# Kernel tuning notes

Measured on AMD Instinct MI355X. Metric: run time of the kernel, lower is better.

## Reference

```python
import jax, jax.numpy as jnp
import numpy as np

D_IN = 1024
D_OUT = 1024
NUM_HEADS = 16
HEAD_DIM = D_OUT // NUM_HEADS


def setup_inputs() -> dict:
    key = jax.random.key(0)
    k_x, k_qkv, k_pw, k_pb = jax.random.split(key, 4)
    x = jax.random.normal(k_x, (2, 2048, D_IN), dtype=jnp.float32)
    # torch nn.Linear(d_in, 3*d_out, bias=False): weight [3*d_out, d_in]
    w_qkv = jax.random.normal(k_qkv, (3 * D_OUT, D_IN), dtype=jnp.float32) * (1.0 / np.sqrt(D_IN))
    # proj: nn.Linear(d_out, d_out) with bias
    w_proj = jax.random.normal(k_pw, (D_OUT, D_OUT), dtype=jnp.float32) * (1.0 / np.sqrt(D_OUT))
    b_proj = jax.random.normal(k_pb, (D_OUT,), dtype=jnp.float32) * 0.01
    return {"x": x, "w_qkv": w_qkv, "w_proj": w_proj, "b_proj": b_proj}


def reference(x, w_qkv, w_proj, b_proj):
    B, S, _ = x.shape
    # fused QKV projection: [B,S,3*D_OUT]
    qkv = jnp.einsum('bsd,ed->bse', x, w_qkv)
    qkv = qkv.reshape(B, S, 3, NUM_HEADS, HEAD_DIM)
    q, k, v = jnp.moveaxis(qkv, 2, 0)  # each [B,S,H,Dh]
    scale = 1.0 / jnp.sqrt(jnp.asarray(HEAD_DIM, dtype=x.dtype))
    # scores [B,H,S,S]
    scores = jnp.einsum('bqhd,bkhd->bhqk', q, k) * scale
    causal = jnp.tril(jnp.ones((S, S), dtype=bool))
    scores = jnp.where(causal, scores, jnp.asarray(-jnp.inf, dtype=scores.dtype))
    attn = jax.nn.softmax(scores, axis=-1)
    ctx = jnp.einsum('bhqk,bkhd->bqhd', attn, v)  # [B,S,H,Dh]
    ctx = ctx.reshape(B, S, D_OUT)
    return jnp.einsum('bsd,ed->bse', ctx, w_proj) + b_proj
```

## Files before the change

### kernel.cpp

```cpp
#include <hip/hip_runtime.h>
#include <hip/hip_bf16.h>
#include <cstdint>

#define B_SZ   2
#define S_LEN  2048
#define NH     16
#define LDA    72

using f32x4 = __attribute__((ext_vector_type(4))) float;
typedef __bf16 bf16x8 __attribute__((ext_vector_type(8)));
typedef __bf16 bf16x4 __attribute__((ext_vector_type(4)));

__device__ inline float bf2f(unsigned short u) {
    union { unsigned int i; float f; } v; v.i = ((unsigned int)u) << 16; return v.f;
}
__device__ inline unsigned short f2bf(float f) {
    union { float f; unsigned int i; } v; v.f = f;
    unsigned int r = v.i + 0x7fff + ((v.i >> 16) & 1);
    return (unsigned short)(r >> 16);
}
__device__ inline f32x4 mfma16(bf16x8 a, bf16x8 b, f32x4 c) {
    return __builtin_amdgcn_mfma_f32_16x16x32_bf16(a, b, c, 0, 0, 0);
}
__device__ inline unsigned pack_bf16x2(float lo, float hi) {
    float2 f2; f2.x = lo; f2.y = hi;
    __hip_bfloat162 bb = __float22bfloat162_rn(f2);
    union { __hip_bfloat162 b; unsigned u; } cv; cv.b = bb;
    return cv.u;
}
__device__ inline void ldsbar() {
    __builtin_amdgcn_sched_barrier(0);
    asm volatile("s_waitcnt lgkmcnt(0)" ::: "memory");
    __builtin_amdgcn_s_barrier();
    __builtin_amdgcn_sched_barrier(0);
}
__device__ inline void stC(float* C, size_t idx, float v)  { C[idx] = v; }
__device__ inline void stC(__bf16* C, size_t idx, float v) { ((unsigned short*)C)[idx] = f2bf(v); }

#define QSF (0.125f * 1.4426950408889634f)

__global__ __launch_bounds__(256) void f2b3_kernel(
    const float* __restrict__ a, int na4, __bf16* __restrict__ outa,
    const float* __restrict__ b, int nb4, __bf16* __restrict__ outb,
    const float* __restrict__ c, int nc4, __bf16* __restrict__ outc)
{
    int i = blockIdx.x * blockDim.x + threadIdx.x;
    const float* src; __bf16* dst; int idx;
    if (i < na4)                  { src = a; dst = outa; idx = i; }
    else if (i < na4 + nb4)       { src = b; dst = outb; idx = i - na4; }
    else if (i < na4 + nb4 + nc4) { src = c; dst = outc; idx = i - na4 - nb4; }
    else return;
    float4 v = ((const float4*)src)[idx];
    ushort4 o;
    o.x = f2bf(v.x); o.y = f2bf(v.y); o.z = f2bf(v.z); o.w = f2bf(v.w);
    ((ushort4*)dst)[idx] = o;
}

template <typename TO, int HAS_BIAS, int QSCALE>
__global__ __launch_bounds__(256) void gemm128(
    const __bf16* __restrict__ A, const __bf16* __restrict__ W,
    const float* __restrict__ bias, TO* __restrict__ C,
    int M, int N, int K)
{
    __shared__ __bf16 Alds[3][128 * 32];
    __shared__ __bf16 Blds[3][128 * 32];
    const int tid  = threadIdx.x, lane = tid & 63, w = tid >> 6;
    const int c16  = lane & 15, quad = lane >> 4;
    const int mBase = blockIdx.y * 128, nBase = blockIdx.x * 128;
    const int moff = (w & 1) * 64, noff = (w >> 1) * 64;

    f32x4 acc[4][4];
#pragma unroll
    for (int i = 0; i < 4; ++i)
#pragma unroll
        for (int j = 0; j < 4; ++j) acc[i][j] = (f32x4){0.f, 0.f, 0.f, 0.f};

    auto stage = [&](int buf, int k0) {
#pragma unroll
        for (int p = 0; p < 2; ++p) {
            const int linear = p * 256 + tid;
            const int row = linear >> 2;
            const int seg = (linear & 3) ^ (row & 3);
            const int lbase = (p * 256 + w * 64) * 8;
            const __bf16* ga = A + (size_t)(mBase + row) * K + k0 + seg * 8;
            const __bf16* gb = W + (size_t)(nBase + row) * K + k0 + seg * 8;
            __builtin_amdgcn_global_load_lds(
                (const __attribute__((address_space(1))) void*)ga,
                (__attribute__((address_space(3))) void*)(&Alds[buf][lbase]), 16, 0, 0);
            __builtin_amdgcn_global_load_lds(
                (const __attribute__((address_space(1))) void*)gb,
                (__attribute__((address_space(3))) void*)(&Blds[buf][lbase]), 16, 0, 0);
        }
    };

    stage(0, 0);
    if (32 < K) stage(1, 32);
    int cur = 0;
    for (int k0 = 0; k0 < K; k0 += 32) {
        __builtin_amdgcn_sched_barrier(0);
        if (k0 + 32 < K) asm volatile("s_waitcnt vmcnt(4) lgkmcnt(0)" ::: "memory");
        else             asm volatile("s_waitcnt vmcnt(0) lgkmcnt(0)" ::: "memory");
        __builtin_amdgcn_s_barrier();
        __builtin_amdgcn_sched_barrier(0);

        if (k0 + 64 < K) stage(cur == 0 ? 2 : cur - 1, k0 + 64);

        bf16x8 af[4], bw[4];
#pragma unroll
        for (int i = 0; i < 4; ++i) {
            const int rowA = moff + i * 16 + c16;
            af[i] = *(const bf16x8*)&Alds[cur][rowA * 32 + ((quad ^ (rowA & 3)) << 3)];
            const int rowB = noff + i * 16 + c16;
            bw[i] = *(const bf16x8*)&Blds[cur][rowB * 32 + ((quad ^ (rowB & 3)) << 3)];
        }
#pragma unroll
        for (int i = 0; i < 4; ++i)
#pragma unroll
            for (int j = 0; j < 4; ++j)
                acc[i][j] = mfma16(af[i], bw[j], acc[i][j]);
        cur = (cur == 2) ? 0 : cur + 1;
    }

#pragma unroll
    for (int j = 0; j < 4; ++j) {
        const int colBase = nBase + noff + j * 16;
        const float qs = (QSCALE && colBase < 1024) ? QSF : 1.0f;
        const int col = colBase + c16;
        const float bv = HAS_BIAS ? bias[col] : 0.f;
#pragma unroll
        for (int i = 0; i < 4; ++i)
#pragma unroll
            for (int r = 0; r < 4; ++r) {
                const int row = mBase + moff + i * 16 + quad * 4 + r;
                stC(C, (size_t)row * N + col, acc[i][j][r] * qs + bv);
            }
    }
}

template <typename TO, int HAS_BIAS>
__global__ __launch_bounds__(256) void gemm64(
    const __bf16* __restrict__ A, const __bf16* __restrict__ W,
    const float* __restrict__ bias, TO* __restrict__ C,
    int M, int N, int K)
{
    __shared__ __bf16 Alds[3][64 * 32];
    __shared__ __bf16 Blds[3][128 * 32];
    const int tid  = threadIdx.x, lane = tid & 63, w = tid >> 6;
    const int c16  = lane & 15, quad = lane >> 4;
    const int mBase = blockIdx.y * 64, nBase = blockIdx.x * 128;
    const int moff = (w & 1) * 32, noff = (w >> 1) * 64;

    f32x4 acc[2][4];
#pragma unroll
    for (int i = 0; i < 2; ++i)
#pragma unroll
        for (int j = 0; j < 4; ++j) acc[i][j] = (f32x4){0.f, 0.f, 0.f, 0.f};

    auto stage = [&](int buf, int k0) {
        {
            const int row = tid >> 2;
            const int seg = (tid & 3) ^ (row & 3);
            const int lbase = (w * 64) * 8;
            const __bf16* ga = A + (size_t)(mBase + row) * K + k0 + seg * 8;
            __builtin_amdgcn_global_load_lds(
                (const __attribute__((address_space(1))) void*)ga,
                (__attribute__((address_space(3))) void*)(&Alds[buf][lbase]), 16, 0, 0);
        }
#pragma unroll
        for (int p = 0; p < 2; ++p) {
            const int linear = p * 256 + tid;
            const int row = linear >> 2;
            const int seg = (linear & 3) ^ (row & 3);
            const int lbase = (p * 256 + w * 64) * 8;
            const __bf16* gb = W + (size_t)(nBase + row) * K + k0 + seg * 8;
            __builtin_amdgcn_global_load_lds(
                (const __attribute__((address_space(1))) void*)gb,
                (__attribute__((address_space(3))) void*)(&Blds[buf][lbase]), 16, 0, 0);
        }
    };

    stage(0, 0);
    if (32 < K) stage(1, 32);
    int cur = 0;
    for (int k0 = 0; k0 < K; k0 += 32) {
        __builtin_amdgcn_sched_barrier(0);
        if (k0 + 32 < K) asm volatile("s_waitcnt vmcnt(3) lgkmcnt(0)" ::: "memory");
        else             asm volatile("s_waitcnt vmcnt(0) lgkmcnt(0)" ::: "memory");
        __builtin_amdgcn_s_barrier();
        __builtin_amdgcn_sched_barrier(0);

        if (k0 + 64 < K) stage(cur == 0 ? 2 : cur - 1, k0 + 64);

        bf16x8 af[2], bw[4];
#pragma unroll
        for (int i = 0; i < 2; ++i) {
            const int rowA = moff + i * 16 + c16;
            af[i] = *(const bf16x8*)&Alds[cur][rowA * 32 + ((quad ^ (rowA & 3)) << 3)];
        }
#pragma unroll
        for (int j = 0; j < 4; ++j) {
            const int rowB = noff + j * 16 + c16;
            bw[j] = *(const bf16x8*)&Blds[cur][rowB * 32 + ((quad ^ (rowB & 3)) << 3)];
        }
#pragma unroll
        for (int i = 0; i < 2; ++i)
#pragma unroll
            for (int j = 0; j < 4; ++j)
                acc[i][j] = mfma16(af[i], bw[j], acc[i][j]);
        cur = (cur == 2) ? 0 : cur + 1;
    }

#pragma unroll
    for (int j = 0; j < 4; ++j) {
        const int col = nBase + noff + j * 16 + c16;
        const float bv = HAS_BIAS ? bias[col] : 0.f;
#pragma unroll
        for (int i = 0; i < 2; ++i)
#pragma unroll
            for (int r = 0; r < 4; ++r) {
                const int row = mBase + moff + i * 16 + quad * 4 + r;
                stC(C, (size_t)row * N + col, acc[i][j][r] + bv);
            }
    }
}

__global__ __launch_bounds__(256) void attn(
    const __bf16* __restrict__ qkv, __bf16* __restrict__ ctx)
{
    __shared__ __bf16 Ks[2][64 * LDA];
    __shared__ __bf16 Vs[2][64 * LDA];

    const int tid  = threadIdx.x;
    const int lane = tid & 63;
    const int w    = tid >> 6;
    const int c16  = lane & 15;
    const int quad = lane >> 4;
    const int bh = blockIdx.x, b = bh >> 4, h = bh & 15;
    const int y  = blockIdx.y;

    const int a  = y & 7, uq = y >> 3;
    const int qt = (uq == 0) ? (31 - a) : (uq == 1) ? (16 + a)
                 : (uq == 2) ? (15 - a) : a;
    const int c1 = qt + 1;
    const int qBase = qt * 64;

    const int krow0 = tid >> 3;
    const int kd0   = (tid & 7) * 8;
    const int u     = tid & 31;
    const int dblk  = tid >> 5;
    const int vcol  = 32 * (u & 1) + 8 * ((u >> 1) & 3) + 2 * (u >> 3);

    const size_t rowB = (size_t)b * S_LEN;

    const __bf16* kp0 = qkv + (rowB + krow0) * 3072 + 1024 + h * 64 + kd0;
    const __bf16* kp1 = kp0 + (size_t)32 * 3072;
    const __bf16* vp0 = qkv + (rowB + 2 * u) * 3072 + 2048 + h * 64 + dblk * 8;
    const __bf16* vp1 = vp0 + (size_t)3072;

    uint4 kr0 = *(const uint4*)kp0;
    uint4 kr1 = *(const uint4*)kp1;
    uint4 vr0 = *(const uint4*)vp0;
    uint4 vr1 = *(const uint4*)vp1;

    const __bf16* qp = qkv + (rowB + qBase + w * 16 + c16) * 3072 + h * 64;
    const bf16x8 aq0 = *(const bf16x8*)(qp + quad * 8);
    const bf16x8 aq1 = *(const bf16x8*)(qp + 32 + quad * 8);

    auto stageKV = [&](int buf) {
        *(uint4*)&Ks[buf][krow0 * LDA + kd0]        = kr0;
        *(uint4*)&Ks[buf][(krow0 + 32) * LDA + kd0] = kr1;
        const unsigned short* e1 = (const unsigned short*)&vr0;
        const unsigned short* e2 = (const unsigned short*)&vr1;
#pragma unroll
        for (int d = 0; d < 8; ++d) {
            const unsigned pack = (unsigned)e1[d] | ((unsigned)e2[d] << 16);
            *(unsigned*)&Vs[buf][(dblk * 8 + d) * LDA + vcol] = pack;
        }
    };
    auto loadNext = [&]() {
        kp0 += (size_t)64 * 3072; kp1 += (size_t)64 * 3072;
        vp0 += (size_t)64 * 3072; vp1 += (size_t)64 * 3072;
        kr0 = *(const uint4*)kp0;
        kr1 = *(const uint4*)kp1;
        vr0 = *(const uint4*)vp0;
        vr1 = *(const uint4*)vp1;
    };

    stageKV(0);
    if (1 < c1) loadNext();
    ldsbar();

    float lp = 0.f;
    f32x4 acc_o[4];
#pragma unroll
    for (int j = 0; j < 4; ++j) acc_o[j] = (f32x4){0.f, 0.f, 0.f, 0.f};

    for (int cc = 0; cc < c1; ++cc) {
        const int cur = cc & 1;
        if (cc + 1 < c1) {
            stageKV(cur ^ 1);
            if (cc + 2 < c1) loadNext();
        }

        f32x4 sc[4];
#pragma unroll
        for (int j = 0; j < 4; ++j) sc[j] = (f32x4){0.f, 0.f, 0.f, 0.f};
#pragma unroll
        for (int j = 0; j < 4; ++j) {
            bf16x8 bk0 = *(const bf16x8*)&Ks[cur][(j * 16 + c16) * LDA + quad * 8];
            bf16x8 bk1 = *(const bf16x8*)&Ks[cur][(j * 16 + c16) * LDA + 32 + quad * 8];
            sc[j] = mfma16(bk0, aq0, sc[j]);
            sc[j] = mfma16(bk1, aq1, sc[j]);
        }

        if (cc == qt) {
            const int q = qBase + w * 16 + c16;
#pragma unroll
            for (int j = 0; j < 4; ++j) {
#pragma unroll
                for (int r = 0; r < 4; ++r) {
                    const int key = cc * 64 + j * 16 + quad * 4 + r;
                    if (key > q) sc[j][r] = -1e30f;
                }
            }
        }

        float p_[4][4];
#pragma unroll
        for (int j = 0; j < 4; ++j)
#pragma unroll
            for (int r = 0; r < 4; ++r)
                p_[j][r] = exp2f(sc[j][r]);
#pragma unroll
        for (int j = 0; j < 4; ++j)
            lp += (p_[j][0] + p_[j][1]) + (p_[j][2] + p_[j][3]);

        union { unsigned uu[4]; bf16x8 v; } B0, B1;
#pragma unroll
        for (int j = 0; j < 4; ++j) {
            B0.uu[j] = pack_bf16x2(p_[j][0], p_[j][1]);
            B1.uu[j] = pack_bf16x2(p_[j][2], p_[j][3]);
        }
        const bf16x8 bp0 = B0.v;
        const bf16x8 bp1 = B1.v;

#pragma unroll
        for (int jd = 0; jd < 4; ++jd) {
            bf16x8 av0 = *(const bf16x8*)&Vs[cur][(jd * 16 + c16) * LDA + quad * 8];
            bf16x8 av1 = *(const bf16x8*)&Vs[cur][(jd * 16 + c16) * LDA + 32 + quad * 8];
            acc_o[jd] = mfma16(av0, bp0, acc_o[jd]);
            acc_o[jd] = mfma16(av1, bp1, acc_o[jd]);
        }
        ldsbar();
    }

    lp += __shfl_xor(lp, 16);
    lp += __shfl_xor(lp, 32);

    const float inv = 1.0f / lp;
    const size_t rowO = (rowB + qBase + w * 16 + c16) * 1024 + h * 64;
#pragma unroll
    for (int jd = 0; jd < 4; ++jd) {
        bf16x4 ov;
#pragma unroll
        for (int r = 0; r < 4; ++r) ov[r] = (__bf16)(acc_o[jd][r] * inv);
        *(bf16x4*)&ctx[rowO + jd * 16 + quad * 4] = ov;
    }
}

extern "C" void kernel_launch(void* const* d_in, const int* in_sizes, int n_in,
                              void* d_out, int out_size, void* d_ws, size_t ws_size,
                              hipStream_t stream) {
    const float* x      = (const float*)d_in[0];
    const float* w_qkv  = (const float*)d_in[1];
    const float* w_proj = (const float*)d_in[2];
    const float* b_proj = (const float*)d_in[3];
    float* out = (float*)d_out;

    __bf16* qkvb = (__bf16*)d_ws;
    __bf16* xb   = qkvb + (size_t)4096 * 3072;
    __bf16* wqb  = xb + (size_t)4096 * 1024;
    __bf16* wpb  = wqb + (size_t)3072 * 1024;
    __bf16* ctxb = xb;

    const int M = B_SZ * S_LEN;
    const int nx4 = 4096 * 1024 / 4, nq4 = 3072 * 1024 / 4, np4 = 1024 * 1024 / 4;

    f2b3_kernel<<<(nx4 + nq4 + np4 + 255) / 256, 256, 0, stream>>>(
        x, nx4, xb, w_qkv, nq4, wqb, w_proj, np4, wpb);

    gemm128<__bf16, 0, 1><<<dim3(3072 / 128, M / 128), 256, 0, stream>>>(
        xb, wqb, nullptr, qkvb, M, 3072, 1024);

    attn<<<dim3(B_SZ * NH, 32), 256, 0, stream>>>(qkvb, ctxb);

    gemm64<float, 1><<<dim3(1024 / 128, M / 64), 256, 0, stream>>>(
        ctxb, wpb, b_proj, out, M, 1024, 1024);
}
```

Before: 179.8 us.

## Single-buffer K/V in LDS, stage Q via LDS, add MFMA priority hints

Replaces the double-buffered K/V shared-memory tiles with a single buffer. Each iteration now stores its tile, synchronises, and then prefetches the next tile into registers, which adds a second barrier per iteration. Q is loaded cooperatively through LDS with coalesced loads instead of per-lane global loads. The MFMA sections are wrapped in s_setprio so waves issue matrix ops ahead of others. Total LDS use drops from 4 tiles to 3, which may raise occupancy, at the cost of extra synchronisation.

```diff
diff --git a/kernel.cpp b/kernel.cpp
--- a/kernel.cpp
+++ b/kernel.cpp
@@ -227,8 +227,9 @@
 __global__ __launch_bounds__(256) void attn(
     const __bf16* __restrict__ qkv, __bf16* __restrict__ ctx)
 {
-    __shared__ __bf16 Ks[2][64 * LDA];
-    __shared__ __bf16 Vs[2][64 * LDA];
+    __shared__ __bf16 Qs[64 * LDA];
+    __shared__ __bf16 Ks[64 * LDA];
+    __shared__ __bf16 Vs[64 * LDA];
 
     const int tid  = threadIdx.x;
     const int lane = tid & 63;
@@ -262,33 +263,18 @@
     uint4 vr0 = *(const uint4*)vp0;
     uint4 vr1 = *(const uint4*)vp1;
 
-    const __bf16* qp = qkv + (rowB + qBase + w * 16 + c16) * 3072 + h * 64;
-    const bf16x8 aq0 = *(const bf16x8*)(qp + quad * 8);
-    const bf16x8 aq1 = *(const bf16x8*)(qp + 32 + quad * 8);
-
-    auto stageKV = [&](int buf) {
-        *(uint4*)&Ks[buf][krow0 * LDA + kd0]        = kr0;
-        *(uint4*)&Ks[buf][(krow0 + 32) * LDA + kd0] = kr1;
-        const unsigned short* e1 = (const unsigned short*)&vr0;
-        const unsigned short* e2 = (const unsigned short*)&vr1;
-#pragma unroll
-        for (int d = 0; d < 8; ++d) {
-            const unsigned pack = (unsigned)e1[d] | ((unsigned)e2[d] << 16);
-            *(unsigned*)&Vs[buf][(dblk * 8 + d) * LDA + vcol] = pack;
-        }
-    };
-    auto loadNext = [&]() {
-        kp0 += (size_t)64 * 3072; kp1 += (size_t)64 * 3072;
-        vp0 += (size_t)64 * 3072; vp1 += (size_t)64 * 3072;
-        kr0 = *(const uint4*)kp0;
-        kr1 = *(const uint4*)kp1;
-        vr0 = *(const uint4*)vp0;
-        vr1 = *(const uint4*)vp1;
-    };
-
-    stageKV(0);
-    if (1 < c1) loadNext();
+#pragma unroll
+    for (int p = 0; p < 2; ++p) {
+        const int linear = p * 256 + tid;
+        const int row = linear >> 3;
+        const int d0 = (linear & 7) * 8;
+        const __bf16* g = qkv + (rowB + qBase + row) * 3072 + h * 64 + d0;
+        *(uint4*)&Qs[row * LDA + d0] = *(const uint4*)g;
+    }
     ldsbar();
+
+    const bf16x8 aq0 = *(const bf16x8*)&Qs[(w * 16 + c16) * LDA + quad * 8];
+    const bf16x8 aq1 = *(const bf16x8*)&Qs[(w * 16 + c16) * LDA + 32 + quad * 8];
 
     float lp = 0.f;
     f32x4 acc_o[4];
@@ -296,22 +282,40 @@
     for (int j = 0; j < 4; ++j) acc_o[j] = (f32x4){0.f, 0.f, 0.f, 0.f};
 
     for (int cc = 0; cc < c1; ++cc) {
-        const int cur = cc & 1;
+        *(uint4*)&Ks[krow0 * LDA + kd0]        = kr0;
+        *(uint4*)&Ks[(krow0 + 32) * LDA + kd0] = kr1;
+        {
+            const unsigned short* e1 = (const unsigned short*)&vr0;
+            const unsigned short* e2 = (const unsigned short*)&vr1;
+#pragma unroll
+            for (int d = 0; d < 8; ++d) {
+                const unsigned pack = (unsigned)e1[d] | ((unsigned)e2[d] << 16);
+                *(unsigned*)&Vs[(dblk * 8 + d) * LDA + vcol] = pack;
+            }
+        }
+        ldsbar();
+
         if (cc + 1 < c1) {
-            stageKV(cur ^ 1);
-            if (cc + 2 < c1) loadNext();
+            kp0 += (size_t)64 * 3072; kp1 += (size_t)64 * 3072;
+            vp0 += (size_t)64 * 3072; vp1 += (size_t)64 * 3072;
+            kr0 = *(const uint4*)kp0;
+            kr1 = *(const uint4*)kp1;
+            vr0 = *(const uint4*)vp0;
+            vr1 = *(const uint4*)vp1;
         }
 
         f32x4 sc[4];
 #pragma unroll
         for (int j = 0; j < 4; ++j) sc[j] = (f32x4){0.f, 0.f, 0.f, 0.f};
+        __builtin_amdgcn_s_setprio(1);
 #pragma unroll
         for (int j = 0; j < 4; ++j) {
-            bf16x8 bk0 = *(const bf16x8*)&Ks[cur][(j * 16 + c16) * LDA + quad * 8];
-            bf16x8 bk1 = *(const bf16x8*)&Ks[cur][(j * 16 + c16) * LDA + 32 + quad * 8];
+            bf16x8 bk0 = *(const bf16x8*)&Ks[(j * 16 + c16) * LDA + quad * 8];
+            bf16x8 bk1 = *(const bf16x8*)&Ks[(j * 16 + c16) * LDA + 32 + quad * 8];
             sc[j] = mfma16(bk0, aq0, sc[j]);
             sc[j] = mfma16(bk1, aq1, sc[j]);
         }
+        __builtin_amdgcn_s_setprio(0);
 
         if (cc == qt) {
             const int q = qBase + w * 16 + c16;
@@ -344,13 +348,15 @@
         const bf16x8 bp0 = B0.v;
         const bf16x8 bp1 = B1.v;
 
+        __builtin_amdgcn_s_setprio(1);
 #pragma unroll
         for (int jd = 0; jd < 4; ++jd) {
-            bf16x8 av0 = *(const bf16x8*)&Vs[cur][(jd * 16 + c16) * LDA + quad * 8];
-            bf16x8 av1 = *(const bf16x8*)&Vs[cur][(jd * 16 + c16) * LDA + 32 + quad * 8];
+            bf16x8 av0 = *(const bf16x8*)&Vs[(jd * 16 + c16) * LDA + quad * 8];
+            bf16x8 av1 = *(const bf16x8*)&Vs[(jd * 16 + c16) * LDA + 32 + quad * 8];
             acc_o[jd] = mfma16(av0, bp0, acc_o[jd]);
             acc_o[jd] = mfma16(av1, bp1, acc_o[jd]);
         }
+        __builtin_amdgcn_s_setprio(0);
         ldsbar();
     }
 
```

Result: faster. 175.0 us (-2.6%).
